# Kernel tuning notes

Measured on AMD Instinct MI355X. Metric: run time of the kernel, lower is better.

Reference implementation:

```python
import math
import jax, jax.numpy as jnp
import numpy as np

B, T, D_MODEL, HEAD_DIM = 4, 2048, 768, 64

def setup_inputs() -> dict:
    key = jax.random.key(0)
    ks = jax.random.split(key, 4)
    scale = 1.0 / math.sqrt(D_MODEL)
    return {
        "x": jax.random.normal(ks[0], (B, T, D_MODEL), dtype=jnp.float32),
        "Wq": jax.random.normal(ks[1], (D_MODEL, HEAD_DIM), dtype=jnp.float32) * scale,
        "bq": jnp.zeros((HEAD_DIM,), dtype=jnp.float32),
        "Wk": jax.random.normal(ks[2], (D_MODEL, HEAD_DIM), dtype=jnp.float32) * scale,
        "bk": jnp.zeros((HEAD_DIM,), dtype=jnp.float32),
        "Wv": jax.random.normal(ks[3], (D_MODEL, HEAD_DIM), dtype=jnp.float32) * scale,
        "bv": jnp.zeros((HEAD_DIM,), dtype=jnp.float32),
    }

def reference(x, Wq, bq, Wk, bk, Wv, bv):
    # Single causal self-attention head (dropout=0 / eval mode).
    q = x @ Wq + bq                      # [B, T, H]
    k = x @ Wk + bk                      # [B, T, H]
    v = x @ Wv + bv                      # [B, T, H]
    head_dim = q.shape[-1]
    scores = jnp.einsum("bth,bsh->bts", q, k) / math.sqrt(head_dim)  # [B, T, T]
    seq_len = x.shape[1]
    causal = jnp.tril(jnp.ones((seq_len, seq_len), dtype=bool))      # [T, T]
    scores = jnp.where(causal, scores, -jnp.inf)
    attn = jax.nn.softmax(scores, axis=-1)                           # [B, T, T]
    out = jnp.einsum("bts,bsh->bth", attn, v)                        # [B, T, H]
    return out
```

## Files before the change

### kernel.cpp

```cpp
#include <hip/hip_runtime.h>
#include <math.h>

#define BB 4
#define TT 2048
#define DM 768
#define HD 64
#define NROW (BB*TT)
#define WFRAG_HALF ((size_t)24*12*512)

typedef __attribute__((ext_vector_type(8))) short bf16x8;
typedef __attribute__((ext_vector_type(4))) float f32x4;

__device__ __forceinline__ unsigned short f2bf(float f) {
    unsigned int u = __float_as_uint(f);
    u += 0x7FFFu + ((u >> 16) & 1u);
    return (unsigned short)(u >> 16);
}
__device__ __forceinline__ float bf2f(unsigned short h) {
    return __uint_as_float(((unsigned int)h) << 16);
}

__device__ __forceinline__ void g2lds16(const unsigned short* g, unsigned short* l) {
    __builtin_amdgcn_global_load_lds(
        (const __attribute__((address_space(1))) unsigned int*)g,
        (__attribute__((address_space(3))) unsigned int*)l, 16, 0, 0);
}

__global__ __launch_bounds__(256) void wconv_kernel(
    const float* __restrict__ Wq, const float* __restrict__ Wk,
    const float* __restrict__ Wv, unsigned short* __restrict__ wfrag)
{
    __shared__ float ws[32][69];
    const int blk = blockIdx.x;
    const int m = blk / 24, kc = blk % 24;
    const float* Wm = (m == 0) ? Wq : ((m == 1) ? Wk : Wv);
    const float sc = (m == 0) ? 0.125f : 1.0f;
    const int tid = threadIdx.x;
    {
        int r = tid >> 3, c0 = (tid & 7) * 8;
        *(float4*)&ws[r][c0]     = *(const float4*)(Wm + (size_t)(32*kc + r)*HD + c0);
        *(float4*)&ws[r][c0 + 4] = *(const float4*)(Wm + (size_t)(32*kc + r)*HD + c0 + 4);
    }
    __syncthreads();
    const int ntm = tid >> 6, lane = tid & 63;
    const int q15 = lane & 15, g = lane >> 4;
    const int col = 16*ntm + q15;
    bf16x8 hi, lo;
    #pragma unroll
    for (int j = 0; j < 8; ++j) {
        float w = ws[8*g + j][col] * sc;
        unsigned short h = f2bf(w);
        hi[j] = (short)h;
        lo[j] = (short)f2bf(w - bf2f(h));
    }
    size_t base = ((size_t)(kc*12 + m*4 + ntm))*512 + (size_t)lane*8;
    *(bf16x8*)(wfrag + base) = hi;
    *(bf16x8*)(wfrag + WFRAG_HALF + base) = lo;
}

__global__ __launch_bounds__(512) void proj_mfma_kernel(
    const float* __restrict__ x, const unsigned short* __restrict__ wfrag,
    const float* __restrict__ bq, const float* __restrict__ bk,
    const float* __restrict__ bv,
    unsigned short* __restrict__ qo, unsigned short* __restrict__ ko,
    unsigned short* __restrict__ vT)
{
    __shared__ unsigned short xsh[2][32][776];
    __shared__ unsigned short wsh[2][24*512];
    const int tid  = threadIdx.x;
    const int wv   = tid >> 6;
    const int lane = tid & 63;
    const int q15  = lane & 15;
    const int g    = lane >> 4;
    const int row0 = blockIdx.x * 32;
    const int mt   = wv & 1;
    const int nt0  = 3 * (wv >> 1);
    const int xrow = 16*mt + q15;

    {
        const int r  = tid >> 4;
        const int c4 = (tid & 15) * 4;
        const float* xp = x + (size_t)(row0 + r)*DM + c4;
        #pragma unroll
        for (int p = 0; p < 12; ++p) {
            float4 xv = *(const float4*)(xp + 64*p);
            float f[4] = {xv.x, xv.y, xv.z, xv.w};
            ushort4 hi, lo;
            unsigned short h;
            h = f2bf(f[0]); hi.x = h; lo.x = f2bf(f[0] - bf2f(h));
            h = f2bf(f[1]); hi.y = h; lo.y = f2bf(f[1] - bf2f(h));
            h = f2bf(f[2]); hi.z = h; lo.z = f2bf(f[2] - bf2f(h));
            h = f2bf(f[3]); hi.w = h; lo.w = f2bf(f[3] - bf2f(h));
            *(ushort4*)&xsh[0][r][c4 + 64*p] = hi;
            *(ushort4*)&xsh[1][r][c4 + 64*p] = lo;
        }
    }
    #pragma unroll
    for (int jj = 0; jj < 3; ++jj) {
        int j = 3*wv + jj;
        const unsigned short* src = wfrag
            + (j < 12 ? (size_t)j*512 : WFRAG_HALF + (size_t)(j - 12)*512)
            + (size_t)lane*8;
        g2lds16(src, &wsh[0][j*512]);
    }
    __syncthreads();

    f32x4 acc[3];
    #pragma unroll
    for (int i = 0; i < 3; ++i) acc[i] = (f32x4){0.f, 0.f, 0.f, 0.f};

    for (int kcg = 0; kcg < 24; ++kcg) {
        const int buf = kcg & 1;
        if (kcg < 23) {
            const int kn = kcg + 1;
            #pragma unroll
            for (int jj = 0; jj < 3; ++jj) {
                int j = 3*wv + jj;
                const unsigned short* src = wfrag
                    + (j < 12 ? (size_t)(kn*12 + j)*512
                              : WFRAG_HALF + (size_t)(kn*12 + j - 12)*512)
                    + (size_t)lane*8;
                g2lds16(src, &wsh[buf^1][j*512]);
            }
        }
        bf16x8 xfh = *(const bf16x8*)&xsh[0][xrow][kcg*32 + 8*g];
        bf16x8 xfl = *(const bf16x8*)&xsh[1][xrow][kcg*32 + 8*g];
        #pragma unroll
        for (int i = 0; i < 3; ++i) {
            const int nt = nt0 + i;
            bf16x8 wh = *(const bf16x8*)&wsh[buf][nt*512 + lane*8];
            bf16x8 wl = *(const bf16x8*)&wsh[buf][(12 + nt)*512 + lane*8];
            acc[i] = __builtin_amdgcn_mfma_f32_16x16x32_bf16(xfh, wh, acc[i], 0, 0, 0);
            acc[i] = __builtin_amdgcn_mfma_f32_16x16x32_bf16(xfl, wh, acc[i], 0, 0, 0);
            acc[i] = __builtin_amdgcn_mfma_f32_16x16x32_bf16(xfh, wl, acc[i], 0, 0, 0);
        }
        __syncthreads();
    }

    const int b  = row0 >> 11;
    const int t0 = row0 & 2047;
    #pragma unroll
    for (int i = 0; i < 3; ++i) {
        int nt = nt0 + i, m = nt >> 2, ntm = nt & 3;
        int col = 16*ntm + q15;
        float bb = (m == 0) ? 0.125f*bq[col] : ((m == 1) ? bk[col] : bv[col]);
        if (m == 2) {
            ushort4 pk;
            pk.x = f2bf(acc[i][0] + bb);
            pk.y = f2bf(acc[i][1] + bb);
            pk.z = f2bf(acc[i][2] + bb);
            pk.w = f2bf(acc[i][3] + bb);
            *(ushort4*)(vT + ((size_t)b*HD + col)*TT + t0 + 16*mt + 4*g) = pk;
        } else {
            unsigned short* op = (m == 0) ? qo : ko;
            #pragma unroll
            for (int r = 0; r < 4; ++r)
                op[(size_t)(row0 + 16*mt + 4*g + r)*HD + col] = f2bf(acc[i][r] + bb);
        }
    }
}

__global__ __launch_bounds__(256) void attn_mfma_kernel(
    const unsigned short* __restrict__ qb_, const unsigned short* __restrict__ kb_,
    const unsigned short* __restrict__ vt_, float* __restrict__ out)
{
    __shared__ unsigned short plds[4][16][40];
    __shared__ float olds[4][16][66];
    __shared__ float mlds[4][16][2];

    const int tid  = threadIdx.x;
    const int wv   = tid >> 6;
    const int lane = tid & 63;
    const int q15  = lane & 15;
    const int g    = lane >> 4;

    const int bx = blockIdx.x;
    const int b  = bx & 3;
    const int qt = (TT/16 - 1) - (bx >> 2);
    const int qbase = qt * 16;
    const int nk = qbase + 16;

    const unsigned short* qp = qb_ + (size_t)b*TT*HD;
    const unsigned short* kp = kb_ + (size_t)b*TT*HD;
    const unsigned short* vp = vt_ + (size_t)b*HD*TT;

    bf16x8 qf[2];
    #pragma unroll
    for (int c = 0; c < 2; ++c)
        qf[c] = *(const bf16x8*)(qp + (size_t)(qbase + q15)*HD + 32*c + 8*g);

    f32x4 accv[4];
    #pragma unroll
    for (int h = 0; h < 4; ++h) accv[h] = (f32x4){0.f, 0.f, 0.f, 0.f};
    float m = -INFINITY, l = 0.f;

    const int ck = ((nk + 127) >> 7) << 5;
    const int kstart = wv * ck;
    const int kend = min(kstart + ck, nk);

    for (int k0 = kstart; k0 < kend; k0 += 32) {
        bf16x8 vf[4];
        #pragma unroll
        for (int h = 0; h < 4; ++h)
            vf[h] = *(const bf16x8*)(vp + (size_t)(16*h + q15)*TT + k0 + 8*g);
        bf16x8 kf[2][2];
        #pragma unroll
        for (int t = 0; t < 2; ++t)
            #pragma unroll
            for (int c = 0; c < 2; ++c)
                kf[t][c] = *(const bf16x8*)(kp + (size_t)(k0 + 16*t + q15)*HD + 32*c + 8*g);

        f32x4 st[2];
        #pragma unroll
        for (int t = 0; t < 2; ++t) {
            f32x4 z = {0.f, 0.f, 0.f, 0.f};
            st[t] = __builtin_amdgcn_mfma_f32_16x16x32_bf16(kf[t][0], qf[0], z, 0, 0, 0);
            st[t] = __builtin_amdgcn_mfma_f32_16x16x32_bf16(kf[t][1], qf[1], st[t], 0, 0, 0);
        }
        if (k0 + 31 > qbase) {
            int qabs = qbase + q15;
            #pragma unroll
            for (int t = 0; t < 2; ++t)
                #pragma unroll
                for (int r = 0; r < 4; ++r)
                    if (k0 + 16*t + 4*g + r > qabs) st[t][r] = -INFINITY;
        }
        float pmax = st[0][0];
        #pragma unroll
        for (int t = 0; t < 2; ++t)
            #pragma unroll
            for (int r = 0; r < 4; ++r) pmax = fmaxf(pmax, st[t][r]);
        pmax = fmaxf(pmax, __shfl_xor(pmax, 16));
        pmax = fmaxf(pmax, __shfl_xor(pmax, 32));
        float mnew = fmaxf(m, pmax);
        float mc = fmaxf(mnew, -1e30f);
        float alpha = __expf(m - mc);
        float p[2][4];
        float psum = 0.f;
        #pragma unroll
        for (int t = 0; t < 2; ++t)
            #pragma unroll
            for (int r = 0; r < 4; ++r) {
                p[t][r] = __expf(st[t][r] - mc);
                psum += p[t][r];
            }
        psum += __shfl_xor(psum, 16);
        psum += __shfl_xor(psum, 32);
        l = l * alpha + psum;
        m = mnew;
        float av[4];
        #pragma unroll
        for (int r = 0; r < 4; ++r) av[r] = __shfl(alpha, 4*g + r);
        #pragma unroll
        for (int h = 0; h < 4; ++h)
            #pragma unroll
            for (int r = 0; r < 4; ++r) accv[h][r] *= av[r];
        #pragma unroll
        for (int t = 0; t < 2; ++t) {
            ushort4 pk;
            pk.x = f2bf(p[t][0]); pk.y = f2bf(p[t][1]);
            pk.z = f2bf(p[t][2]); pk.w = f2bf(p[t][3]);
            *(ushort4*)&plds[wv][q15][16*t + 4*g] = pk;
        }
        bf16x8 pa = *(const bf16x8*)&plds[wv][q15][8*g];
        #pragma unroll
        for (int h = 0; h < 4; ++h)
            accv[h] = __builtin_amdgcn_mfma_f32_16x16x32_bf16(pa, vf[h], accv[h], 0, 0, 0);
    }

    #pragma unroll
    for (int h = 0; h < 4; ++h)
        #pragma unroll
        for (int r = 0; r < 4; ++r)
            olds[wv][4*g + r][16*h + q15] = accv[h][r];
    if (g == 0) { mlds[wv][q15][0] = m; mlds[wv][q15][1] = l; }
    __syncthreads();

    {
        int qq = tid >> 4;
        int c4 = (tid & 15) << 2;
        float mw[4], lw[4];
        #pragma unroll
        for (int w = 0; w < 4; ++w) { mw[w] = mlds[w][qq][0]; lw[w] = mlds[w][qq][1]; }
        float M = fmaxf(fmaxf(mw[0], mw[1]), fmaxf(mw[2], mw[3]));
        float Mc = fmaxf(M, -1e30f);
        float ww[4], ltot = 0.f;
        #pragma unroll
        for (int w = 0; w < 4; ++w) { ww[w] = __expf(mw[w] - Mc); ltot += ww[w]*lw[w]; }
        float invl = 1.f / ltot;
        float4 o;
        #pragma unroll
        for (int e = 0; e < 4; ++e) {
            float s = 0.f;
            #pragma unroll
            for (int w = 0; w < 4; ++w) s += ww[w] * olds[w][qq][c4 + e];
            ((float*)&o)[e] = s * invl;
        }
        *(float4*)(out + ((size_t)b*TT + qbase + qq)*HD + c4) = o;
    }
}

extern "C" void kernel_launch(void* const* d_in, const int* in_sizes, int n_in,
                              void* d_out, int out_size, void* d_ws, size_t ws_size,
                              hipStream_t stream) {
    const float* x  = (const float*)d_in[0];
    const float* Wq = (const float*)d_in[1];
    const float* bq = (const float*)d_in[2];
    const float* Wk = (const float*)d_in[3];
    const float* bk = (const float*)d_in[4];
    const float* Wv = (const float*)d_in[5];
    const float* bv = (const float*)d_in[6];
    float* out = (float*)d_out;

    unsigned short* qbf   = (unsigned short*)d_ws;
    unsigned short* kbf   = qbf + (size_t)NROW*HD;
    unsigned short* vT    = kbf + (size_t)NROW*HD;
    unsigned short* wfrag = vT  + (size_t)NROW*HD;

    wconv_kernel<<<72, 256, 0, stream>>>(Wq, Wk, Wv, wfrag);
    proj_mfma_kernel<<<NROW/32, 512, 0, stream>>>(x, wfrag, bq, bk, bv, qbf, kbf, vT);
    attn_mfma_kernel<<<dim3(TT/16 * BB), 256, 0, stream>>>(qbf, kbf, vT, out);
}
```

Before: 55.40 us.

## Load weight fragments directly to registers and stage projection outputs through LDS

The projection kernel no longer stages weight fragments in LDS with global_load_lds double buffering. Each wave now prefetches its own next-k weight fragments from global memory into registers, which removes the per-iteration __syncthreads. The epilogue first writes Q/K/V results into the reused x shared buffer, then stores them to global memory with coalesced vector writes instead of scattered 2-byte stores. The cost is higher register pressure, and weight traffic now goes through the cache path per wave instead of being shared across the block.

```diff
diff --git a/kernel.cpp b/kernel.cpp
--- a/kernel.cpp
+++ b/kernel.cpp
@@ -18,12 +18,6 @@
 }
 __device__ __forceinline__ float bf2f(unsigned short h) {
     return __uint_as_float(((unsigned int)h) << 16);
-}
-
-__device__ __forceinline__ void g2lds16(const unsigned short* g, unsigned short* l) {
-    __builtin_amdgcn_global_load_lds(
-        (const __attribute__((address_space(1))) unsigned int*)g,
-        (__attribute__((address_space(3))) unsigned int*)l, 16, 0, 0);
 }
 
 __global__ __launch_bounds__(256) void wconv_kernel(
@@ -66,7 +60,6 @@
     unsigned short* __restrict__ vT)
 {
     __shared__ unsigned short xsh[2][32][776];
-    __shared__ unsigned short wsh[2][24*512];
     const int tid  = threadIdx.x;
     const int wv   = tid >> 6;
     const int lane = tid & 63;
@@ -95,68 +88,80 @@
             *(ushort4*)&xsh[1][r][c4 + 64*p] = lo;
         }
     }
-    #pragma unroll
-    for (int jj = 0; jj < 3; ++jj) {
-        int j = 3*wv + jj;
-        const unsigned short* src = wfrag
-            + (j < 12 ? (size_t)j*512 : WFRAG_HALF + (size_t)(j - 12)*512)
-            + (size_t)lane*8;
-        g2lds16(src, &wsh[0][j*512]);
-    }
     __syncthreads();
 
     f32x4 acc[3];
     #pragma unroll
     for (int i = 0; i < 3; ++i) acc[i] = (f32x4){0.f, 0.f, 0.f, 0.f};
 
+    bf16x8 wch[3], wcl[3];
+    #pragma unroll
+    for (int i = 0; i < 3; ++i) {
+        const unsigned short* wp = wfrag + ((size_t)(nt0 + i))*512 + (size_t)lane*8;
+        wch[i] = *(const bf16x8*)wp;
+        wcl[i] = *(const bf16x8*)(wp + WFRAG_HALF);
+    }
     for (int kcg = 0; kcg < 24; ++kcg) {
-        const int buf = kcg & 1;
+        bf16x8 wnh[3], wnl[3];
         if (kcg < 23) {
-            const int kn = kcg + 1;
-            #pragma unroll
-            for (int jj = 0; jj < 3; ++jj) {
-                int j = 3*wv + jj;
-                const unsigned short* src = wfrag
-                    + (j < 12 ? (size_t)(kn*12 + j)*512
-                              : WFRAG_HALF + (size_t)(kn*12 + j - 12)*512)
-                    + (size_t)lane*8;
-                g2lds16(src, &wsh[buf^1][j*512]);
+            #pragma unroll
+            for (int i = 0; i < 3; ++i) {
+                const unsigned short* wp = wfrag
+                    + ((size_t)((kcg + 1)*12 + nt0 + i))*512 + (size_t)lane*8;
+                wnh[i] = *(const bf16x8*)wp;
+                wnl[i] = *(const bf16x8*)(wp + WFRAG_HALF);
             }
         }
         bf16x8 xfh = *(const bf16x8*)&xsh[0][xrow][kcg*32 + 8*g];
         bf16x8 xfl = *(const bf16x8*)&xsh[1][xrow][kcg*32 + 8*g];
         #pragma unroll
         for (int i = 0; i < 3; ++i) {
-            const int nt = nt0 + i;
-            bf16x8 wh = *(const bf16x8*)&wsh[buf][nt*512 + lane*8];
-            bf16x8 wl = *(const bf16x8*)&wsh[buf][(12 + nt)*512 + lane*8];
-            acc[i] = __builtin_amdgcn_mfma_f32_16x16x32_bf16(xfh, wh, acc[i], 0, 0, 0);
-            acc[i] = __builtin_amdgcn_mfma_f32_16x16x32_bf16(xfl, wh, acc[i], 0, 0, 0);
-            acc[i] = __builtin_amdgcn_mfma_f32_16x16x32_bf16(xfh, wl, acc[i], 0, 0, 0);
-        }
-        __syncthreads();
-    }
-
-    const int b  = row0 >> 11;
-    const int t0 = row0 & 2047;
+            acc[i] = __builtin_amdgcn_mfma_f32_16x16x32_bf16(xfh, wch[i], acc[i], 0, 0, 0);
+            acc[i] = __builtin_amdgcn_mfma_f32_16x16x32_bf16(xfl, wch[i], acc[i], 0, 0, 0);
+            acc[i] = __builtin_amdgcn_mfma_f32_16x16x32_bf16(xfh, wcl[i], acc[i], 0, 0, 0);
+        }
+        #pragma unroll
+        for (int i = 0; i < 3; ++i) { wch[i] = wnh[i]; wcl[i] = wnl[i]; }
+    }
+
+    __syncthreads();
+    unsigned short* sqk = (unsigned short*)xsh;
+    unsigned short* sv  = sqk + 2*32*72;
     #pragma unroll
     for (int i = 0; i < 3; ++i) {
         int nt = nt0 + i, m = nt >> 2, ntm = nt & 3;
         int col = 16*ntm + q15;
         float bb = (m == 0) ? 0.125f*bq[col] : ((m == 1) ? bk[col] : bv[col]);
+        unsigned short pk[4];
+        #pragma unroll
+        for (int r = 0; r < 4; ++r) pk[r] = f2bf(acc[i][r] + bb);
         if (m == 2) {
-            ushort4 pk;
-            pk.x = f2bf(acc[i][0] + bb);
-            pk.y = f2bf(acc[i][1] + bb);
-            pk.z = f2bf(acc[i][2] + bb);
-            pk.w = f2bf(acc[i][3] + bb);
-            *(ushort4*)(vT + ((size_t)b*HD + col)*TT + t0 + 16*mt + 4*g) = pk;
+            ushort4 v4 = make_ushort4(pk[0], pk[1], pk[2], pk[3]);
+            *(ushort4*)&sv[(size_t)col*36 + 16*mt + 4*g] = v4;
         } else {
-            unsigned short* op = (m == 0) ? qo : ko;
             #pragma unroll
             for (int r = 0; r < 4; ++r)
-                op[(size_t)(row0 + 16*mt + 4*g + r)*HD + col] = f2bf(acc[i][r] + bb);
-        }
+                sqk[((size_t)m*32 + 16*mt + 4*g + r)*72 + col] = pk[r];
+        }
+    }
+    __syncthreads();
+    {
+        const int mqk = tid >> 8;
+        const int rr  = (tid >> 3) & 31;
+        const int c8  = (tid & 7) * 8;
+        unsigned short* op = (mqk == 0) ? qo : ko;
+        ushort4 a = *(const ushort4*)&sqk[((size_t)mqk*32 + rr)*72 + c8];
+        ushort4 bqk = *(const ushort4*)&sqk[((size_t)mqk*32 + rr)*72 + c8 + 4];
+        *(ushort4*)(op + (size_t)(row0 + rr)*HD + c8)     = a;
+        *(ushort4*)(op + (size_t)(row0 + rr)*HD + c8 + 4) = bqk;
+    }
+    {
+        const int col = tid >> 3;
+        const int tg  = (tid & 7) * 4;
+        const int b   = row0 >> 11;
+        const int t0  = row0 & 2047;
+        ushort4 v4 = *(const ushort4*)&sv[(size_t)col*36 + tg];
+        *(ushort4*)(vT + ((size_t)b*HD + col)*TT + t0 + tg) = v4;
     }
 }
 
```

Result: slower. 57.90 us (+4.5%).

## Restructure QKV projection: column-group blocks hold full weight slice in LDS

Applied to the files above, without the earlier changes.

The projection kernel now launches 256 blocks of 256 threads. Each block owns 128 rows and one quarter of the 192 output columns, and loads its whole hi/lo bf16 weight slice (144 KB) into dynamic LDS once, so the per-k-step double-buffered weight loads and barriers go away. x is streamed straight from global memory into registers with a 4-deep prefetch, and the hi/lo split now truncates instead of rounding to nearest, which removes the LDS staging of x. Each wave computes two 16-row tiles so each weight fragment is reused twice. In exchange, every x row is read by four blocks, occupancy drops to one block per CU, and the truncation split slightly changes numerics.

```diff
diff --git a/kernel.cpp b/kernel.cpp
--- a/kernel.cpp
+++ b/kernel.cpp
@@ -53,109 +53,116 @@
         hi[j] = (short)h;
         lo[j] = (short)f2bf(w - bf2f(h));
     }
-    size_t base = ((size_t)(kc*12 + m*4 + ntm))*512 + (size_t)lane*8;
+    size_t base = ((size_t)((m*4 + ntm)*24 + kc))*512 + (size_t)lane*8;
     *(bf16x8*)(wfrag + base) = hi;
     *(bf16x8*)(wfrag + WFRAG_HALF + base) = lo;
 }
 
-__global__ __launch_bounds__(512) void proj_mfma_kernel(
+__global__ __launch_bounds__(256, 1) void proj_mfma_kernel(
     const float* __restrict__ x, const unsigned short* __restrict__ wfrag,
     const float* __restrict__ bq, const float* __restrict__ bk,
     const float* __restrict__ bv,
     unsigned short* __restrict__ qo, unsigned short* __restrict__ ko,
     unsigned short* __restrict__ vT)
 {
-    __shared__ unsigned short xsh[2][32][776];
-    __shared__ unsigned short wsh[2][24*512];
+    extern __shared__ unsigned short wlds[];
     const int tid  = threadIdx.x;
     const int wv   = tid >> 6;
     const int lane = tid & 63;
     const int q15  = lane & 15;
     const int g    = lane >> 4;
-    const int row0 = blockIdx.x * 32;
-    const int mt   = wv & 1;
-    const int nt0  = 3 * (wv >> 1);
-    const int xrow = 16*mt + q15;
-
-    {
-        const int r  = tid >> 4;
-        const int c4 = (tid & 15) * 4;
-        const float* xp = x + (size_t)(row0 + r)*DM + c4;
-        #pragma unroll
-        for (int p = 0; p < 12; ++p) {
-            float4 xv = *(const float4*)(xp + 64*p);
-            float f[4] = {xv.x, xv.y, xv.z, xv.w};
-            ushort4 hi, lo;
-            unsigned short h;
-            h = f2bf(f[0]); hi.x = h; lo.x = f2bf(f[0] - bf2f(h));
-            h = f2bf(f[1]); hi.y = h; lo.y = f2bf(f[1] - bf2f(h));
-            h = f2bf(f[2]); hi.z = h; lo.z = f2bf(f[2] - bf2f(h));
-            h = f2bf(f[3]); hi.w = h; lo.w = f2bf(f[3] - bf2f(h));
-            *(ushort4*)&xsh[0][r][c4 + 64*p] = hi;
-            *(ushort4*)&xsh[1][r][c4 + 64*p] = lo;
-        }
-    }
-    #pragma unroll
-    for (int jj = 0; jj < 3; ++jj) {
-        int j = 3*wv + jj;
-        const unsigned short* src = wfrag
-            + (j < 12 ? (size_t)j*512 : WFRAG_HALF + (size_t)(j - 12)*512)
-            + (size_t)lane*8;
-        g2lds16(src, &wsh[0][j*512]);
+    const int bx   = blockIdx.x;
+    const int ng   = bx & 3;
+    const int rt0  = (bx >> 2) * 128;
+    const int wrow0 = rt0 + 32*wv;
+
+    #pragma unroll
+    for (int j = 0; j < 36; ++j) {
+        const int s = wv*36 + j;
+        const int kcg = s / 6, r6 = s % 6;
+        const int part = r6 / 3, ntl = r6 % 3;
+        const unsigned short* src = wfrag + (size_t)part*WFRAG_HALF
+            + ((size_t)((3*ng + ntl)*24 + kcg))*512 + (size_t)lane*8;
+        g2lds16(src, wlds + (size_t)s*512);
+    }
+
+    const float* xp0 = x + (size_t)(wrow0 + q15)*DM + 8*g;
+    const float* xp1 = x + (size_t)(wrow0 + 16 + q15)*DM + 8*g;
+    float4 pf[4][2][2];
+    #pragma unroll
+    for (int kb = 0; kb < 4; ++kb) {
+        pf[kb][0][0] = *(const float4*)(xp0 + 32*kb);
+        pf[kb][0][1] = *(const float4*)(xp0 + 32*kb + 4);
+        pf[kb][1][0] = *(const float4*)(xp1 + 32*kb);
+        pf[kb][1][1] = *(const float4*)(xp1 + 32*kb + 4);
     }
     __syncthreads();
 
-    f32x4 acc[3];
-    #pragma unroll
-    for (int i = 0; i < 3; ++i) acc[i] = (f32x4){0.f, 0.f, 0.f, 0.f};
-
-    for (int kcg = 0; kcg < 24; ++kcg) {
-        const int buf = kcg & 1;
-        if (kcg < 23) {
-            const int kn = kcg + 1;
-            #pragma unroll
-            for (int jj = 0; jj < 3; ++jj) {
-                int j = 3*wv + jj;
-                const unsigned short* src = wfrag
-                    + (j < 12 ? (size_t)(kn*12 + j)*512
-                              : WFRAG_HALF + (size_t)(kn*12 + j - 12)*512)
-                    + (size_t)lane*8;
-                g2lds16(src, &wsh[buf^1][j*512]);
+    f32x4 acc[2][3];
+    #pragma unroll
+    for (int mt = 0; mt < 2; ++mt)
+        #pragma unroll
+        for (int i = 0; i < 3; ++i) acc[mt][i] = (f32x4){0.f, 0.f, 0.f, 0.f};
+
+    #pragma unroll
+    for (int kb = 0; kb < 24; ++kb) {
+        const int slot = kb & 3;
+        bf16x8 xh[2], xl[2];
+        #pragma unroll
+        for (int mt = 0; mt < 2; ++mt) {
+            float f[8] = {pf[slot][mt][0].x, pf[slot][mt][0].y,
+                          pf[slot][mt][0].z, pf[slot][mt][0].w,
+                          pf[slot][mt][1].x, pf[slot][mt][1].y,
+                          pf[slot][mt][1].z, pf[slot][mt][1].w};
+            #pragma unroll
+            for (int e = 0; e < 8; ++e) {
+                unsigned short h = (unsigned short)(__float_as_uint(f[e]) >> 16);
+                float rr = f[e] - bf2f(h);
+                xh[mt][e] = (short)h;
+                xl[mt][e] = (short)(unsigned short)(__float_as_uint(rr) >> 16);
             }
         }
-        bf16x8 xfh = *(const bf16x8*)&xsh[0][xrow][kcg*32 + 8*g];
-        bf16x8 xfl = *(const bf16x8*)&xsh[1][xrow][kcg*32 + 8*g];
+        if (kb < 20) {
+            pf[slot][0][0] = *(const float4*)(xp0 + 32*(kb+4));
+            pf[slot][0][1] = *(const float4*)(xp0 + 32*(kb+4) + 4);
+            pf[slot][1][0] = *(const float4*)(xp1 + 32*(kb+4));
+            pf[slot][1][1] = *(const float4*)(xp1 + 32*(kb+4) + 4);
+        }
         #pragma unroll
         for (int i = 0; i < 3; ++i) {
-            const int nt = nt0 + i;
-            bf16x8 wh = *(const bf16x8*)&wsh[buf][nt*512 + lane*8];
-            bf16x8 wl = *(const bf16x8*)&wsh[buf][(12 + nt)*512 + lane*8];
-            acc[i] = __builtin_amdgcn_mfma_f32_16x16x32_bf16(xfh, wh, acc[i], 0, 0, 0);
-            acc[i] = __builtin_amdgcn_mfma_f32_16x16x32_bf16(xfl, wh, acc[i], 0, 0, 0);
-            acc[i] = __builtin_amdgcn_mfma_f32_16x16x32_bf16(xfh, wl, acc[i], 0, 0, 0);
-        }
-        __syncthreads();
-    }
-
-    const int b  = row0 >> 11;
-    const int t0 = row0 & 2047;
+            bf16x8 wh = *(const bf16x8*)(wlds + (size_t)(kb*6 + i)*512     + (size_t)lane*8);
+            bf16x8 wl = *(const bf16x8*)(wlds + (size_t)(kb*6 + 3 + i)*512 + (size_t)lane*8);
+            #pragma unroll
+            for (int mt = 0; mt < 2; ++mt) {
+                acc[mt][i] = __builtin_amdgcn_mfma_f32_16x16x32_bf16(xh[mt], wh, acc[mt][i], 0, 0, 0);
+                acc[mt][i] = __builtin_amdgcn_mfma_f32_16x16x32_bf16(xl[mt], wh, acc[mt][i], 0, 0, 0);
+                acc[mt][i] = __builtin_amdgcn_mfma_f32_16x16x32_bf16(xh[mt], wl, acc[mt][i], 0, 0, 0);
+            }
+        }
+    }
+
+    const int b  = wrow0 >> 11;
+    const int t0 = wrow0 & 2047;
     #pragma unroll
     for (int i = 0; i < 3; ++i) {
-        int nt = nt0 + i, m = nt >> 2, ntm = nt & 3;
-        int col = 16*ntm + q15;
-        float bb = (m == 0) ? 0.125f*bq[col] : ((m == 1) ? bk[col] : bv[col]);
-        if (m == 2) {
-            ushort4 pk;
-            pk.x = f2bf(acc[i][0] + bb);
-            pk.y = f2bf(acc[i][1] + bb);
-            pk.z = f2bf(acc[i][2] + bb);
-            pk.w = f2bf(acc[i][3] + bb);
-            *(ushort4*)(vT + ((size_t)b*HD + col)*TT + t0 + 16*mt + 4*g) = pk;
-        } else {
-            unsigned short* op = (m == 0) ? qo : ko;
-            #pragma unroll
-            for (int r = 0; r < 4; ++r)
-                op[(size_t)(row0 + 16*mt + 4*g + r)*HD + col] = f2bf(acc[i][r] + bb);
+        const int nt = 3*ng + i, m = nt >> 2, ntm = nt & 3;
+        const int col = 16*ntm + q15;
+        const float bb = (m == 0) ? 0.125f*bq[col] : ((m == 1) ? bk[col] : bv[col]);
+        #pragma unroll
+        for (int mt = 0; mt < 2; ++mt) {
+            if (m == 2) {
+                ushort4 pk;
+                pk.x = f2bf(acc[mt][i][0] + bb);
+                pk.y = f2bf(acc[mt][i][1] + bb);
+                pk.z = f2bf(acc[mt][i][2] + bb);
+                pk.w = f2bf(acc[mt][i][3] + bb);
+                *(ushort4*)(vT + ((size_t)b*HD + col)*TT + t0 + 16*mt + 4*g) = pk;
+            } else {
+                unsigned short* op = (m == 0) ? qo : ko;
+                #pragma unroll
+                for (int r = 0; r < 4; ++r)
+                    op[(size_t)(wrow0 + 16*mt + 4*g + r)*HD + col] = f2bf(acc[mt][i][r] + bb);
+            }
         }
     }
 }
@@ -317,7 +324,10 @@
     unsigned short* vT    = kbf + (size_t)NROW*HD;
     unsigned short* wfrag = vT  + (size_t)NROW*HD;
 
+    hipFuncSetAttribute((const void*)proj_mfma_kernel,
+                        hipFuncAttributeMaxDynamicSharedMemorySize, 147456);
+
     wconv_kernel<<<72, 256, 0, stream>>>(Wq, Wk, Wv, wfrag);
-    proj_mfma_kernel<<<NROW/32, 512, 0, stream>>>(x, wfrag, bq, bk, bv, qbf, kbf, vT);
+    proj_mfma_kernel<<<256, 256, 147456, stream>>>(x, wfrag, bq, bk, bv, qbf, kbf, vT);
     attn_mfma_kernel<<<dim3(TT/16 * BB), 256, 0, stream>>>(qbf, kbf, vT, out);
 }
```

Result: slower. 59.82 us (+8.0%).
